# Kernel tuning notes

Measured on AMD Instinct MI355X. Metric: run time of the kernel, lower is better.

Reference implementation:

```python
import jax, jax.numpy as jnp
import numpy as np

SEQ, BATCH, IN, H = 2048, 1024, 1, 32


def _lstm_layer(x, Wih, Whh, bih, bhh):
    # x: (T, B, in); Wih: (4H, in); Whh: (4H, H); biases: (4H,)
    T, B = x.shape[0], x.shape[1]
    Hh = Whh.shape[1]
    x_proj = jnp.einsum('tbi,gi->tbg', x, Wih) + bih + bhh  # (T, B, 4H)

    def step(carry, xt):
        h, c = carry
        gates = xt + h @ Whh.T  # (B, 4H)
        i, f, g, o = jnp.split(gates, 4, axis=-1)  # PyTorch gate order i,f,g,o
        i = jax.nn.sigmoid(i)
        f = jax.nn.sigmoid(f)
        g = jnp.tanh(g)
        o = jax.nn.sigmoid(o)
        c = f * c + i * g
        h = o * jnp.tanh(c)
        return (h, c), h

    h0 = jnp.zeros((B, Hh), dtype=x.dtype)
    c0 = jnp.zeros((B, Hh), dtype=x.dtype)
    (_, _), out = jax.lax.scan(step, (h0, c0), x_proj)
    return out  # (T, B, H)


def setup_inputs() -> dict:
    key = jax.random.key(0)
    ks = jax.random.split(key, 16)
    s = 1.0 / np.sqrt(H)  # PyTorch LSTM/Linear init scale
    d = {'x': jax.random.normal(ks[0], (SEQ, BATCH, IN), dtype=jnp.float32)}
    in_dims = [IN, H, H]
    ki = 1
    for l in range(3):
        d[f'Wih{l}'] = jax.random.uniform(ks[ki + 0], (4 * H, in_dims[l]), minval=-s, maxval=s)
        d[f'Whh{l}'] = jax.random.uniform(ks[ki + 1], (4 * H, H), minval=-s, maxval=s)
        d[f'bih{l}'] = jax.random.uniform(ks[ki + 2], (4 * H,), minval=-s, maxval=s)
        d[f'bhh{l}'] = jax.random.uniform(ks[ki + 3], (4 * H,), minval=-s, maxval=s)
        ki += 4
    d['Wfc'] = jax.random.uniform(ks[13], (1, H), minval=-s, maxval=s)
    d['bfc'] = jax.random.uniform(ks[14], (1,), minval=-s, maxval=s)
    return d


def reference(x, Wih0, Whh0, bih0, bhh0, Wih1, Whh1, bih1, bhh1,
              Wih2, Whh2, bih2, bhh2, Wfc, bfc):
    out = _lstm_layer(x, Wih0, Whh0, bih0, bhh0)
    out = _lstm_layer(out, Wih1, Whh1, bih1, bhh1)
    out = _lstm_layer(out, Wih2, Whh2, bih2, bhh2)
    return out @ Wfc.T + bfc  # (T, B, 1)
```

## Files before the change

kernel.cpp:

```cpp
#include <hip/hip_runtime.h>

#define T_STEPS 2048
#define NBATCH  1024
#define L2E     1.442695040888963f

typedef _Float16 f16x8 __attribute__((ext_vector_type(8)));
typedef float    f32x4 __attribute__((ext_vector_type(4)));

__device__ __forceinline__ unsigned pk2(float a, float b) {
    auto v = __builtin_amdgcn_cvt_pkrtz(a, b);
    return __builtin_bit_cast(unsigned, v);
}

__device__ __forceinline__ f16x8 loadrow8(const float* p) {
    float4 lo = *reinterpret_cast<const float4*>(p);
    float4 hi = *reinterpret_cast<const float4*>(p + 4);
    f16x8 r;
    r[0] = (_Float16)lo.x; r[1] = (_Float16)lo.y;
    r[2] = (_Float16)lo.z; r[3] = (_Float16)lo.w;
    r[4] = (_Float16)hi.x; r[5] = (_Float16)hi.y;
    r[6] = (_Float16)hi.z; r[7] = (_Float16)hi.w;
    return r;
}

__device__ __forceinline__ void sync_lds() {
    asm volatile("s_waitcnt lgkmcnt(0)" ::: "memory");
    __builtin_amdgcn_s_barrier();
    asm volatile("" ::: "memory");
}

#define PIN8(f) do { uint4 _u = __builtin_bit_cast(uint4, (f));              \
    asm volatile("" : "+v"(_u.x), "+v"(_u.y), "+v"(_u.z), "+v"(_u.w));       \
    (f) = __builtin_bit_cast(f16x8, _u); } while (0)

__global__ __launch_bounds__(768, 1)
void lstm3_ws12q_kernel(const float* __restrict__ x,
                        const float* __restrict__ Wih0, const float* __restrict__ Whh0,
                        const float* __restrict__ bih0, const float* __restrict__ bhh0,
                        const float* __restrict__ Wih1, const float* __restrict__ Whh1,
                        const float* __restrict__ bih1, const float* __restrict__ bhh1,
                        const float* __restrict__ Wih2, const float* __restrict__ Whh2,
                        const float* __restrict__ bih2, const float* __restrict__ bhh2,
                        const float* __restrict__ Wfc,  const float* __restrict__ bfc,
                        float* __restrict__ out)
{
    const int tid = threadIdx.x;
    const int wid = tid >> 6;
    const int lay = wid >> 2;
    const int q   = wid & 3;
    const int l   = tid & 63;
    const int g   = l >> 4;
    const int b   = l & 15;
    const int qa  = l & 3;
    const int gp  = (l & 15) >> 2;
    const int b0  = blockIdx.x * 16;
    const int m0  = q * 2;

    __shared__ __align__(16) f16x8 hH[3][3][64];
    __shared__ float FCpart[3][3][16];
    __shared__ char  pad[86016];

    f16x8 Fi[2], Fh[2];
    {
        const int rowA = qa * 32 + 8 * gp + m0;
        const float* Pi = (lay == 1) ? Wih1 : ((lay == 2) ? Wih2 : nullptr);
        const float* Ph = (lay == 0) ? Whh0 : ((lay == 1) ? Whh1 : Whh2);
#pragma unroll
        for (int mm = 0; mm < 2; ++mm) {
            Fh[mm] = loadrow8(Ph + (rowA + mm) * 32 + 8 * g);
            PIN8(Fh[mm]);
        }
        if (lay != 0) {
#pragma unroll
            for (int mm = 0; mm < 2; ++mm) {
                Fi[mm] = loadrow8(Pi + (rowA + mm) * 32 + 8 * g);
                PIN8(Fi[mm]);
            }
        }
    }

    float4 bs[2], w0s[2];
    float wfc_r[2];
    {
        const float* BI = (lay == 0) ? bih0 : ((lay == 1) ? bih1 : bih2);
        const float* BH = (lay == 0) ? bhh0 : ((lay == 1) ? bhh1 : bhh2);
#pragma unroll
        for (int mm = 0; mm < 2; ++mm) {
            const int u = 8 * g + m0 + mm;
            const float bx = BI[u]      + BH[u];
            const float by = BI[u + 32] + BH[u + 32];
            const float bz = BI[u + 64] + BH[u + 64];
            const float bw = BI[u + 96] + BH[u + 96];
            bs[mm] = make_float4(-L2E * bx, -L2E * by, 2.f * L2E * bz, -L2E * bw);
            if (lay == 0)
                w0s[mm] = make_float4(-L2E * Wih0[u],          -L2E * Wih0[u + 32],
                                      2.f * L2E * Wih0[u + 64], -L2E * Wih0[u + 96]);
            if (lay == 2) wfc_r[mm] = Wfc[u];
        }
    }
    const float bfc0 = bfc[0];

    if (bfc0 == 1e30f) { pad[tid] = 1; out[0] = pad[0]; }

    if (q == 0) {
        f16x8 zz = {0, 0, 0, 0, 0, 0, 0, 0};
        hH[0][lay][l] = zz; hH[1][lay][l] = zz; hH[2][lay][l] = zz;
    }
    if (lay == 2 && q == 0 && l < 16) {
        FCpart[0][0][l] = 0.f; FCpart[0][1][l] = 0.f; FCpart[0][2][l] = 0.f;
        FCpart[1][0][l] = 0.f; FCpart[1][1][l] = 0.f; FCpart[1][2][l] = 0.f;
        FCpart[2][0][l] = 0.f; FCpart[2][1][l] = 0.f; FCpart[2][2][l] = 0.f;
    }
    __syncthreads();

    float cst[2] = {0.f, 0.f};
    float vprev = 0.f;
    float xv = (lay == 0) ? x[b0 + b] : 0.f;

#define ACT2(USE_X, XV)                                                      \
    do {                                                                     \
        _Pragma("unroll")                                                    \
        for (int mm = 0; mm < 2; ++mm) {                                     \
            float ti = fmaf(-L2E,      acc[mm][0], bs[mm].x);                \
            float tf = fmaf(-L2E,      acc[mm][1], bs[mm].y);                \
            float tg = fmaf(2.f * L2E, acc[mm][2], bs[mm].z);                \
            float to = fmaf(-L2E,      acc[mm][3], bs[mm].w);                \
            if (USE_X) {                                                     \
                ti = fmaf(w0s[mm].x, (XV), ti);                              \
                tf = fmaf(w0s[mm].y, (XV), tf);                              \
                tg = fmaf(w0s[mm].z, (XV), tg);                              \
                to = fmaf(w0s[mm].w, (XV), to);                              \
            }                                                                \
            const float ei = __builtin_amdgcn_exp2f(ti);                     \
            const float ef = __builtin_amdgcn_exp2f(tf);                     \
            const float eg = __builtin_amdgcn_exp2f(tg);                     \
            const float eo = __builtin_amdgcn_exp2f(to);                     \
            const float ig = (eg - 1.f) *                                    \
                __builtin_amdgcn_rcpf((1.f + ei) * (1.f + eg));              \
            const float ff = __builtin_amdgcn_rcpf(1.f + ef);                \
            cst[mm] = fmaf(ff, cst[mm], ig);                                 \
            const float tc = fminf(2.f * L2E * cst[mm], 60.f);               \
            const float ec = __builtin_amdgcn_exp2f(tc);                     \
            hn[mm] = (ec - 1.f) *                                            \
                __builtin_amdgcn_rcpf((1.f + eo) * (1.f + ec));              \
        }                                                                    \
    } while (0)

    const int NIT = T_STEPS + 3;
    int sw = 0, sp = 2;
    for (int n = 0; n < NIT; ++n) {
        f32x4 acc[2];
        float hn[2];
        if (lay == 0) {
            if (n < T_STEPS) {
                const int tn = (n + 1 < T_STEPS) ? n + 1 : T_STEPS - 1;
                const float xn = x[tn * NBATCH + b0 + b];
                const f16x8 hb0 = hH[sp][0][l];
#pragma unroll
                for (int mm = 0; mm < 2; ++mm) {
                    f32x4 z = {0.f, 0.f, 0.f, 0.f};
                    acc[mm] = __builtin_amdgcn_mfma_f32_16x16x32_f16(Fh[mm], hb0, z, 0, 0, 0);
                }
                ACT2(1, xv);
                reinterpret_cast<unsigned*>(&hH[sw][0][l])[q] = pk2(hn[0], hn[1]);
                xv = xn;
            }
        } else if (lay == 1) {
            if (n >= 1 && n <= T_STEPS) {
                const f16x8 hb0 = hH[sp][0][l];
                const f16x8 hb1 = hH[sp][1][l];
#pragma unroll
                for (int mm = 0; mm < 2; ++mm) {
                    f32x4 z = {0.f, 0.f, 0.f, 0.f};
                    z       = __builtin_amdgcn_mfma_f32_16x16x32_f16(Fi[mm], hb0, z, 0, 0, 0);
                    acc[mm] = __builtin_amdgcn_mfma_f32_16x16x32_f16(Fh[mm], hb1, z, 0, 0, 0);
                }
                ACT2(0, 0.f);
                reinterpret_cast<unsigned*>(&hH[sw][1][l])[q] = pk2(hn[0], hn[1]);
            }
        } else {
            if (q == 3 && n >= 3 && l < 16)
                out[(n - 3) * NBATCH + b0 + l] =
                    FCpart[sp][0][l] + FCpart[sp][1][l] + FCpart[sp][2][l]
                    + vprev + bfc0;
            if (n >= 2 && n <= T_STEPS + 1) {
                const f16x8 hb1 = hH[sp][1][l];
                const f16x8 hb2 = hH[sp][2][l];
#pragma unroll
                for (int mm = 0; mm < 2; ++mm) {
                    f32x4 z = {0.f, 0.f, 0.f, 0.f};
                    z       = __builtin_amdgcn_mfma_f32_16x16x32_f16(Fi[mm], hb1, z, 0, 0, 0);
                    acc[mm] = __builtin_amdgcn_mfma_f32_16x16x32_f16(Fh[mm], hb2, z, 0, 0, 0);
                }
                ACT2(0, 0.f);
                reinterpret_cast<unsigned*>(&hH[sw][2][l])[q] = pk2(hn[0], hn[1]);
                float v = fmaf(wfc_r[0], hn[0], wfc_r[1] * hn[1]);
                v += __shfl_xor(v, 16);
                v += __shfl_xor(v, 32);
                if (q < 3) { if (l < 16) FCpart[sw][q][l] = v; }
                else       { vprev = v; }
            }
        }

        sync_lds();
        sp = sw; sw = (sw == 2) ? 0 : sw + 1;
    }
#undef ACT2
}

extern "C" void kernel_launch(void* const* d_in, const int* in_sizes, int n_in,
                              void* d_out, int out_size, void* d_ws, size_t ws_size,
                              hipStream_t stream)
{
    const float* x    = (const float*)d_in[0];
    const float* Wih0 = (const float*)d_in[1];
    const float* Whh0 = (const float*)d_in[2];
    const float* bih0 = (const float*)d_in[3];
    const float* bhh0 = (const float*)d_in[4];
    const float* Wih1 = (const float*)d_in[5];
    const float* Whh1 = (const float*)d_in[6];
    const float* bih1 = (const float*)d_in[7];
    const float* bhh1 = (const float*)d_in[8];
    const float* Wih2 = (const float*)d_in[9];
    const float* Whh2 = (const float*)d_in[10];
    const float* bih2 = (const float*)d_in[11];
    const float* bhh2 = (const float*)d_in[12];
    const float* Wfc  = (const float*)d_in[13];
    const float* bfc  = (const float*)d_in[14];
    float* out        = (float*)d_out;

    lstm3_ws12q_kernel<<<dim3(NBATCH / 16), dim3(768), 0, stream>>>(
        x, Wih0, Whh0, bih0, bhh0,
        Wih1, Whh1, bih1, bhh1,
        Wih2, Whh2, bih2, bhh2,
        Wfc, bfc, out);
}
```

Measured before the change: 1.248 ms.

## Split LDS hidden-state layout by quarter and prefetch input-layer h one step early

```diff
diff --git a/kernel.cpp b/kernel.cpp
--- a/kernel.cpp
+++ b/kernel.cpp
@@ -34,7 +34,7 @@
     (f) = __builtin_bit_cast(f16x8, _u); } while (0)
 
 __global__ __launch_bounds__(768, 1)
-void lstm3_ws12q_kernel(const float* __restrict__ x,
+void lstm3_ws12s_kernel(const float* __restrict__ x,
                         const float* __restrict__ Wih0, const float* __restrict__ Whh0,
                         const float* __restrict__ bih0, const float* __restrict__ bhh0,
                         const float* __restrict__ Wih1, const float* __restrict__ Whh1,
@@ -56,7 +56,7 @@
     const int b0  = blockIdx.x * 16;
     const int m0  = q * 2;
 
-    __shared__ __align__(16) f16x8 hH[3][3][64];
+    __shared__ unsigned hS[3][3][4][64];
     __shared__ float FCpart[3][3][16];
     __shared__ char  pad[86016];
 
@@ -103,8 +103,11 @@
     if (bfc0 == 1e30f) { pad[tid] = 1; out[0] = pad[0]; }
 
     if (q == 0) {
-        f16x8 zz = {0, 0, 0, 0, 0, 0, 0, 0};
-        hH[0][lay][l] = zz; hH[1][lay][l] = zz; hH[2][lay][l] = zz;
+#pragma unroll
+        for (int s = 0; s < 3; ++s) {
+            hS[s][lay][0][l] = 0u; hS[s][lay][1][l] = 0u;
+            hS[s][lay][2][l] = 0u; hS[s][lay][3][l] = 0u;
+        }
     }
     if (lay == 2 && q == 0 && l < 16) {
         FCpart[0][0][l] = 0.f; FCpart[0][1][l] = 0.f; FCpart[0][2][l] = 0.f;
@@ -116,6 +119,8 @@
     float cst[2] = {0.f, 0.f};
     float vprev = 0.f;
     float xv = (lay == 0) ? x[b0 + b] : 0.f;
+    f16x8 curH0 = {0, 0, 0, 0, 0, 0, 0, 0};
+    f16x8 curH1 = {0, 0, 0, 0, 0, 0, 0, 0};
 
 #define ACT2(USE_X, XV)                                                      \
     do {                                                                     \
@@ -146,7 +151,13 @@
         }                                                                    \
     } while (0)
 
-    const int NIT = T_STEPS + 3;
+#define RD4(dst, S, LY)                                                      \
+    do { uint4 _u;                                                           \
+        _u.x = hS[S][LY][0][l]; _u.y = hS[S][LY][1][l];                      \
+        _u.z = hS[S][LY][2][l]; _u.w = hS[S][LY][3][l];                      \
+        dst = __builtin_bit_cast(f16x8, _u); } while (0)
+
+    const int NIT = T_STEPS + 5;
     int sw = 0, sp = 2;
     for (int n = 0; n < NIT; ++n) {
         f32x4 acc[2];
@@ -155,57 +166,65 @@
             if (n < T_STEPS) {
                 const int tn = (n + 1 < T_STEPS) ? n + 1 : T_STEPS - 1;
                 const float xn = x[tn * NBATCH + b0 + b];
-                const f16x8 hb0 = hH[sp][0][l];
+                f16x8 hb0;
+                RD4(hb0, sp, 0);
 #pragma unroll
                 for (int mm = 0; mm < 2; ++mm) {
                     f32x4 z = {0.f, 0.f, 0.f, 0.f};
                     acc[mm] = __builtin_amdgcn_mfma_f32_16x16x32_f16(Fh[mm], hb0, z, 0, 0, 0);
                 }
                 ACT2(1, xv);
-                reinterpret_cast<unsigned*>(&hH[sw][0][l])[q] = pk2(hn[0], hn[1]);
+                hS[sw][0][q][l] = pk2(hn[0], hn[1]);
                 xv = xn;
             }
         } else if (lay == 1) {
-            if (n >= 1 && n <= T_STEPS) {
-                const f16x8 hb0 = hH[sp][0][l];
-                const f16x8 hb1 = hH[sp][1][l];
+            f16x8 nxtH0;
+            RD4(nxtH0, sp, 0);
+            if (n >= 2 && n <= T_STEPS + 1) {
+                f16x8 hb1;
+                RD4(hb1, sp, 1);
 #pragma unroll
                 for (int mm = 0; mm < 2; ++mm) {
                     f32x4 z = {0.f, 0.f, 0.f, 0.f};
-                    z       = __builtin_amdgcn_mfma_f32_16x16x32_f16(Fi[mm], hb0, z, 0, 0, 0);
+                    z       = __builtin_amdgcn_mfma_f32_16x16x32_f16(Fi[mm], curH0, z, 0, 0, 0);
                     acc[mm] = __builtin_amdgcn_mfma_f32_16x16x32_f16(Fh[mm], hb1, z, 0, 0, 0);
                 }
                 ACT2(0, 0.f);
-                reinterpret_cast<unsigned*>(&hH[sw][1][l])[q] = pk2(hn[0], hn[1]);
-            }
+                hS[sw][1][q][l] = pk2(hn[0], hn[1]);
+            }
+            curH0 = nxtH0;
         } else {
-            if (q == 3 && n >= 3 && l < 16)
-                out[(n - 3) * NBATCH + b0 + l] =
+            f16x8 nxtH1;
+            RD4(nxtH1, sp, 1);
+            if (q == 3 && n >= 5 && l < 16)
+                out[(n - 5) * NBATCH + b0 + l] =
                     FCpart[sp][0][l] + FCpart[sp][1][l] + FCpart[sp][2][l]
                     + vprev + bfc0;
-            if (n >= 2 && n <= T_STEPS + 1) {
-                const f16x8 hb1 = hH[sp][1][l];
-                const f16x8 hb2 = hH[sp][2][l];
+            if (n >= 4 && n <= T_STEPS + 3) {
+                f16x8 hb2;
+                RD4(hb2, sp, 2);
 #pragma unroll
                 for (int mm = 0; mm < 2; ++mm) {
                     f32x4 z = {0.f, 0.f, 0.f, 0.f};
-                    z       = __builtin_amdgcn_mfma_f32_16x16x32_f16(Fi[mm], hb1, z, 0, 0, 0);
+                    z       = __builtin_amdgcn_mfma_f32_16x16x32_f16(Fi[mm], curH1, z, 0, 0, 0);
                     acc[mm] = __builtin_amdgcn_mfma_f32_16x16x32_f16(Fh[mm], hb2, z, 0, 0, 0);
                 }
                 ACT2(0, 0.f);
-                reinterpret_cast<unsigned*>(&hH[sw][2][l])[q] = pk2(hn[0], hn[1]);
+                hS[sw][2][q][l] = pk2(hn[0], hn[1]);
                 float v = fmaf(wfc_r[0], hn[0], wfc_r[1] * hn[1]);
                 v += __shfl_xor(v, 16);
                 v += __shfl_xor(v, 32);
                 if (q < 3) { if (l < 16) FCpart[sw][q][l] = v; }
                 else       { vprev = v; }
             }
+            curH1 = nxtH1;
         }
 
         sync_lds();
         sp = sw; sw = (sw == 2) ? 0 : sw + 1;
     }
 #undef ACT2
+#undef RD4
 }
 
 extern "C" void kernel_launch(void* const* d_in, const int* in_sizes, int n_in,
@@ -229,7 +248,7 @@
     const float* bfc  = (const float*)d_in[14];
     float* out        = (float*)d_out;
 
-    lstm3_ws12q_kernel<<<dim3(NBATCH / 16), dim3(768), 0, stream>>>(
+    lstm3_ws12s_kernel<<<dim3(NBATCH / 16), dim3(768), 0, stream>>>(
         x, Wih0, Whh0, bih0, bhh0,
         Wih1, Whh1, bih1, bhh1,
         Wih2, Whh2, bih2, bhh2,
```

Result: slower. 1.318 ms (+5.6%).
